# Kernel optimization log

Measured on AMD Instinct MI355X. Metric: run time of the kernel, lower is better.

Reference implementation:

```python
import jax, jax.numpy as jnp
import numpy as np

B, NU, NT = 128, 32, 64          # batch, users/sample, antennas/sample
IN_F, H, OUT_F, NL = 128, 128, 16, 2
N_U, N_A = B * NU, B * NT        # total user / antenna nodes


def setup_inputs() -> dict:
    key = jax.random.key(0)
    ks = iter(jax.random.split(key, 40))
    p = lambda shape: jax.random.normal(next(ks), shape, jnp.float32) * 0.05
    inp = {
        'user_feat': jax.random.normal(next(ks), (N_U, IN_F), jnp.float32),
        'ant_noise': jax.random.normal(next(ks), (N_A, H), jnp.float32),
    }
    # complete bipartite edges within each batch sample
    b = np.arange(B)[:, None, None]
    u = np.arange(NU)[None, :, None]
    t = np.arange(NT)[None, None, :]
    su = np.broadcast_to(b * NU + u, (B, NU, NT)).reshape(-1)  # user global ids
    dt = np.broadcast_to(b * NT + t, (B, NU, NT)).reshape(-1)  # antenna global ids
    inp['src_u2a'] = jnp.asarray(su, jnp.int32)
    inp['dst_u2a'] = jnp.asarray(dt, jnp.int32)
    inp['src_a2u'] = jnp.asarray(dt, jnp.int32)
    inp['dst_a2u'] = jnp.asarray(su, jnp.int32)
    inp['W_ue'] = p((IN_F, H)); inp['b_ue'] = p((H,))
    inp['W_t'] = p((H, H));     inp['b_t'] = p((H,))
    for name in ['ca_aggr', 'ca_self', 'ca_comb', 'cu_aggr', 'cu_self', 'cu_comb']:
        inp[name + '_W'] = p((NL, H, H))
        inp[name + '_b'] = p((NL, H))
    inp['W_norm'] = p((H, OUT_F)); inp['b_norm'] = p((OUT_F,))
    return inp


def mlp(x, W, b):
    # stack of NL Linear(H,H) + ReLU, as in MLP module
    for i in range(W.shape[0]):
        x = jax.nn.relu(x @ W[i] + b[i])
    return x


def rel_conv(src_f, dst_f, src_idx, dst_idx, n_dst, aW, ab, sW, sb, cW, cb):
    # GraphConv2: mean-aggregate mlp_aggr(src) over in-edges, combine with mlp_self(dst)
    msg = mlp(src_f, aW, ab)                                   # [n_src, H]
    summed = jax.ops.segment_sum(msg[src_idx], dst_idx, num_segments=n_dst)
    deg = jax.ops.segment_sum(jnp.ones(dst_idx.shape, jnp.float32), dst_idx,
                              num_segments=n_dst)
    mean = summed / jnp.maximum(deg, 1.0)[:, None]
    return mlp(mlp(dst_f, sW, sb) + mean, cW, cb)


def reference(user_feat, ant_noise, src_u2a, dst_u2a, src_a2u, dst_a2u,
              W_ue, b_ue, W_t, b_t,
              ca_aggr_W, ca_aggr_b, ca_self_W, ca_self_b, ca_comb_W, ca_comb_b,
              cu_aggr_W, cu_aggr_b, cu_self_W, cu_self_b, cu_comb_W, cu_comb_b,
              W_norm, b_norm):
    # InitLayer
    hu = jax.nn.relu(user_feat @ W_ue + b_ue)                  # [B*NU, H]
    ant = jax.nn.relu(hu.reshape(B, NU, H).mean(axis=1) @ W_t + b_t)  # [B, H]
    ha = jnp.repeat(ant, NT, axis=0) + ant_noise               # [B*NT, H]
    # two applications of the SAME HeteroGraphConv (shared weights)
    for _ in range(2):
        na = rel_conv(hu, ha, src_u2a, dst_u2a, N_A,
                      ca_aggr_W, ca_aggr_b, ca_self_W, ca_self_b, ca_comb_W, ca_comb_b)
        nu = rel_conv(ha, hu, src_a2u, dst_a2u, N_U,
                      cu_aggr_W, cu_aggr_b, cu_self_W, cu_self_b, cu_comb_W, cu_comb_b)
        hu, ha = nu, na
    # NormLayer: project, split real/imag, normalize to unit modulus
    y = (ha @ W_norm + b_norm).reshape(B, NT, OUT_F)
    rf = OUT_F // 2
    re, im = y[..., :rf], y[..., rf:]
    mag = jnp.sqrt(re * re + im * im)
    return jnp.concatenate([re / mag, im / mag], axis=-1)      # [B, NT, OUT_F]
```

## Files before the change

kernel.cpp:

```cpp
#include <hip/hip_runtime.h>
#include <math.h>


using frag  = __attribute__((ext_vector_type(8))) short;
using f32x4 = __attribute__((ext_vector_type(4))) float;

#define LDST 136
#define SCOPE_AGT __HIP_MEMORY_SCOPE_AGENT

__device__ __forceinline__ float  bf2f(ushort u) { return __uint_as_float(((unsigned)u) << 16); }
__device__ __forceinline__ ushort f2bf(float f) {
    unsigned u = __float_as_uint(f);
    u += 0x7fff + ((u >> 16) & 1);
    return (ushort)(u >> 16);
}
__device__ __forceinline__ void gst4_sc(void* p, unsigned v) {
    asm volatile("global_store_dword %0, %1, off sc1" :: "v"(p), "v"(v) : "memory");
}

struct GP {
    const float *uf, *noise, *b_ue, *W_t, *b_t;
    const float *wsrc[13];
    const float *bias6[6];
    const float *Wn, *bn;
    float *out;
    ushort *WtAll;
    float *pE, *pA0, *pU0, *pA1, *pU1;
    unsigned *cnt, *flg;
};

__device__ __forceinline__ void psync(unsigned* myf, unsigned* pf, unsigned s) {
    asm volatile("s_waitcnt vmcnt(0)" ::: "memory");
    __syncthreads();
    if (threadIdx.x == 0) {
        __hip_atomic_store(myf, s, __ATOMIC_RELAXED, SCOPE_AGT);
        while (__hip_atomic_load(pf, __ATOMIC_RELAXED, SCOPE_AGT) < s)
            __builtin_amdgcn_s_sleep(2);
    }
    __syncthreads();
}

template<int MT, bool MEANADD>
__device__ __forceinline__ void mlp_stage(const ushort* Xl, ushort* Yl,
    const ushort* __restrict__ Wt, const float* __restrict__ bias, const float* meanL)
{
    const int lane = threadIdx.x & 63, wave = threadIdx.x >> 6;
    const int q = lane >> 4, l15 = lane & 15;
    frag A[2][4];
#pragma unroll
    for (int i = 0; i < 2; ++i) {
        const int n0 = (wave * 2 + i) * 16;
#pragma unroll
        for (int kc = 0; kc < 4; ++kc)
            A[i][kc] = *(const frag*)(Wt + (n0 + l15) * 128 + kc * 32 + q * 8);
    }
#pragma unroll
    for (int mt = 0; mt < MT; ++mt) {
        frag Bv[4];
#pragma unroll
        for (int kc = 0; kc < 4; ++kc)
            Bv[kc] = *(const frag*)(Xl + (mt * 16 + l15) * LDST + kc * 32 + q * 8);
#pragma unroll
        for (int i = 0; i < 2; ++i) {
            f32x4 acc = {0.f, 0.f, 0.f, 0.f};
#pragma unroll
            for (int kc = 0; kc < 4; ++kc)
                acc = __builtin_amdgcn_mfma_f32_16x16x32_bf16(A[i][kc], Bv[kc], acc, 0, 0, 0);
            const int n0 = (wave * 2 + i) * 16 + q * 4;
            const float4 bv = *(const float4*)(bias + n0);
            float v0 = acc[0] + bv.x, v1 = acc[1] + bv.y, v2 = acc[2] + bv.z, v3 = acc[3] + bv.w;
            v0 = v0 > 0.f ? v0 : 0.f; v1 = v1 > 0.f ? v1 : 0.f;
            v2 = v2 > 0.f ? v2 : 0.f; v3 = v3 > 0.f ? v3 : 0.f;
            if (MEANADD) {
                const float4 mv = *(const float4*)(meanL + n0);
                v0 += mv.x; v1 += mv.y; v2 += mv.z; v3 += mv.w;
            }
            ushort4 o = { f2bf(v0), f2bf(v1), f2bf(v2), f2bf(v3) };
            *(ushort4*)(Yl + (mt * 16 + l15) * LDST + n0) = o;
        }
    }
}

__device__ __forceinline__ void colsum_sc(const ushort* buf, int rows, float* __restrict__ dst) {
    const int t = threadIdx.x;
    if (t < 128) {
        float s = 0.f;
        for (int r = 0; r < rows; ++r) s += bf2f(buf[r * LDST + t]);
        gst4_sc(dst + t, __float_as_uint(s));
    }
}

__device__ __forceinline__ void wslab(ushort* dst, float* slab,
                                      const float* __restrict__ W, int kb)
{
    for (int c = threadIdx.x; c < 512; c += 256) {
        const int kr = c >> 5, c4 = c & 31;
        const float4 v = *(const float4*)(W + (kb * 16 + kr) * 128 + c4 * 4);
        slab[kr * 129 + c4 * 4 + 0] = v.x; slab[kr * 129 + c4 * 4 + 1] = v.y;
        slab[kr * 129 + c4 * 4 + 2] = v.z; slab[kr * 129 + c4 * 4 + 3] = v.w;
    }
    __syncthreads();
    for (int c = threadIdx.x; c < 1024; c += 256) {
        const int n = c >> 3, k2 = c & 7;
        const unsigned d = (unsigned)f2bf(slab[(2 * k2) * 129 + n])
                         | ((unsigned)f2bf(slab[(2 * k2 + 1) * 129 + n]) << 16);
        gst4_sc(dst + n * 128 + kb * 16 + 2 * k2, d);
    }
    __syncthreads();
}

__global__ __launch_bounds__(256, 1) void k_gnn(GP P)
{
    __shared__ __align__(16) ushort HU [16 * LDST];
    __shared__ __align__(16) ushort HU2[16 * LDST];
    __shared__ __align__(16) ushort HA [32 * LDST];
    __shared__ __align__(16) ushort HA2[32 * LDST];
    __shared__ __align__(16) ushort T0 [32 * LDST];
    __shared__ __align__(16) ushort T1 [32 * LDST];
    __shared__ float meanL[128];
    __shared__ float antL[128];

    const int blk = blockIdx.x, tid = threadIdx.x;
    const int b = blk >> 1, half = blk & 1;
    unsigned* myf = P.flg + blk * 32;
    unsigned* prf = P.flg + (blk ^ 1) * 32;
    const ushort* Wt = P.WtAll;

    if (blk < 104)
        wslab(P.WtAll + (blk >> 3) * 16384, (float*)T1, P.wsrc[blk >> 3], blk & 7);

    for (int c = tid; c < 16 * 32; c += 256) {
        const int r = c >> 5, k4 = c & 31;
        const float4 v = *(const float4*)(P.uf + (size_t)(b * 32 + half * 16 + r) * 128 + k4 * 4);
        ushort4 o = { f2bf(v.x), f2bf(v.y), f2bf(v.z), f2bf(v.w) };
        *(ushort4*)(T0 + r * LDST + k4 * 4) = o;
    }

    asm volatile("s_waitcnt vmcnt(0)" ::: "memory");
    __syncthreads();
    if (tid == 0) {
        if (blk < 104) {
            unsigned old = __hip_atomic_fetch_add(P.cnt, 1u, __ATOMIC_RELAXED, SCOPE_AGT);
            if (old == 103u) __hip_atomic_store(P.cnt + 32, 1u, __ATOMIC_RELAXED, SCOPE_AGT);
        }
        while (__hip_atomic_load(P.cnt + 32, __ATOMIC_RELAXED, SCOPE_AGT) < 1u)
            __builtin_amdgcn_s_sleep(8);
    }
    __syncthreads();

    mlp_stage<1, false>(T0, HU, Wt + 12 * 16384, P.b_ue, nullptr);
    __syncthreads();
    colsum_sc(HU, 16, P.pE + blk * 128);
    psync(myf, prf, 1u);
    if (tid < 128)
        meanL[tid] = (P.pE[blk * 128 + tid] + P.pE[(blk ^ 1) * 128 + tid]) * (1.f / 32.f);
    __syncthreads();
    if (tid < 128) {
        float acc = P.b_t[tid];
#pragma unroll 4
        for (int k = 0; k < 128; ++k) acc += meanL[k] * P.W_t[k * 128 + tid];
        antL[tid] = acc > 0.f ? acc : 0.f;
    }
    __syncthreads();
    for (int c = tid; c < 32 * 32; c += 256) {
        const int r = c >> 5, k4 = c & 31;
        const float4 v = *(const float4*)(P.noise + (size_t)(b * 64 + half * 32 + r) * 128 + k4 * 4);
        ushort4 o = { f2bf(v.x + antL[k4 * 4 + 0]), f2bf(v.y + antL[k4 * 4 + 1]),
                      f2bf(v.z + antL[k4 * 4 + 2]), f2bf(v.w + antL[k4 * 4 + 3]) };
        *(ushort4*)(HA + r * LDST + k4 * 4) = o;
    }
    __syncthreads();

    mlp_stage<1, false>(HU, T0, Wt + 0 * 16384, P.bias6[0], nullptr);
    __syncthreads();
    mlp_stage<1, false>(T0, T1, Wt + 1 * 16384, P.bias6[0] + 128, nullptr);
    __syncthreads();
    colsum_sc(T1, 16, P.pA0 + blk * 128);
    __syncthreads();
    mlp_stage<2, false>(HA, T0, Wt + 6 * 16384, P.bias6[3], nullptr);
    __syncthreads();
    mlp_stage<2, false>(T0, T1, Wt + 7 * 16384, P.bias6[3] + 128, nullptr);
    __syncthreads();
    colsum_sc(T1, 32, P.pU0 + blk * 128);
    psync(myf, prf, 2u);

    if (tid < 128)
        meanL[tid] = (P.pA0[blk * 128 + tid] + P.pA0[(blk ^ 1) * 128 + tid]) * (1.f / 32.f);
    __syncthreads();
    mlp_stage<2, false>(HA, T0, Wt + 2 * 16384, P.bias6[1], nullptr);
    __syncthreads();
    mlp_stage<2, true >(T0, T1, Wt + 3 * 16384, P.bias6[1] + 128, meanL);
    __syncthreads();
    mlp_stage<2, false>(T1, T0, Wt + 4 * 16384, P.bias6[2], nullptr);
    __syncthreads();
    mlp_stage<2, false>(T0, HA2, Wt + 5 * 16384, P.bias6[2] + 128, nullptr);
    __syncthreads();
    if (tid < 128)
        meanL[tid] = (P.pU0[blk * 128 + tid] + P.pU0[(blk ^ 1) * 128 + tid]) * (1.f / 64.f);
    __syncthreads();
    mlp_stage<1, false>(HU, T0, Wt + 8 * 16384, P.bias6[4], nullptr);
    __syncthreads();
    mlp_stage<1, true >(T0, T1, Wt + 9 * 16384, P.bias6[4] + 128, meanL);
    __syncthreads();
    mlp_stage<1, false>(T1, T0, Wt + 10 * 16384, P.bias6[5], nullptr);
    __syncthreads();
    mlp_stage<1, false>(T0, HU2, Wt + 11 * 16384, P.bias6[5] + 128, nullptr);
    __syncthreads();

    mlp_stage<1, false>(HU2, T0, Wt + 0 * 16384, P.bias6[0], nullptr);
    __syncthreads();
    mlp_stage<1, false>(T0, T1, Wt + 1 * 16384, P.bias6[0] + 128, nullptr);
    __syncthreads();
    colsum_sc(T1, 16, P.pA1 + blk * 128);
    __syncthreads();
    mlp_stage<2, false>(HA2, T0, Wt + 6 * 16384, P.bias6[3], nullptr);
    __syncthreads();
    mlp_stage<2, false>(T0, T1, Wt + 7 * 16384, P.bias6[3] + 128, nullptr);
    __syncthreads();
    colsum_sc(T1, 32, P.pU1 + blk * 128);
    psync(myf, prf, 3u);

    if (tid < 128)
        meanL[tid] = (P.pA1[blk * 128 + tid] + P.pA1[(blk ^ 1) * 128 + tid]) * (1.f / 32.f);
    __syncthreads();
    mlp_stage<2, false>(HA2, T0, Wt + 2 * 16384, P.bias6[1], nullptr);
    __syncthreads();
    mlp_stage<2, true >(T0, T1, Wt + 3 * 16384, P.bias6[1] + 128, meanL);
    __syncthreads();
    mlp_stage<2, false>(T1, T0, Wt + 4 * 16384, P.bias6[2], nullptr);
    __syncthreads();
    mlp_stage<2, false>(T0, T1, Wt + 5 * 16384, P.bias6[2] + 128, nullptr);
    __syncthreads();
    float* WnS = (float*)T0;
    for (int c = tid; c < 512; c += 256)
        *(float4*)(WnS + c * 4) = *(const float4*)(P.Wn + c * 4);
    __syncthreads();
    {
        const int row = tid >> 3, j = tid & 7;
        float R = P.bn[j], I = P.bn[j + 8];
        const ushort* h = T1 + row * LDST;
        for (int k = 0; k < 128; ++k) {
            const float hv = bf2f(h[k]);
            R += hv * WnS[k * 16 + j];
            I += hv * WnS[k * 16 + j + 8];
        }
        const float mag = sqrtf(R * R + I * I);
        const int a = b * 64 + half * 32 + row;
        P.out[a * 16 + j]     = R / mag;
        P.out[a * 16 + j + 8] = I / mag;
    }
}

extern "C" void kernel_launch(void* const* d_in, const int* in_sizes, int n_in,
                              void* d_out, int out_size, void* d_ws, size_t ws_size,
                              hipStream_t stream)
{
    GP P;
    P.uf    = (const float*)d_in[0];
    P.noise = (const float*)d_in[1];
    const float* W_ue = (const float*)d_in[6];
    P.b_ue  = (const float*)d_in[7];
    P.W_t   = (const float*)d_in[8];
    P.b_t   = (const float*)d_in[9];
    const float* caW[3] = {(const float*)d_in[10], (const float*)d_in[12], (const float*)d_in[14]};
    const float* cab[3] = {(const float*)d_in[11], (const float*)d_in[13], (const float*)d_in[15]};
    const float* cuW[3] = {(const float*)d_in[16], (const float*)d_in[18], (const float*)d_in[20]};
    const float* cub[3] = {(const float*)d_in[17], (const float*)d_in[19], (const float*)d_in[21]};
    P.Wn  = (const float*)d_in[22];
    P.bn  = (const float*)d_in[23];
    P.out = (float*)d_out;

    P.wsrc[0]  = caW[0]; P.wsrc[1]  = caW[0] + 16384;
    P.wsrc[2]  = caW[1]; P.wsrc[3]  = caW[1] + 16384;
    P.wsrc[4]  = caW[2]; P.wsrc[5]  = caW[2] + 16384;
    P.wsrc[6]  = cuW[0]; P.wsrc[7]  = cuW[0] + 16384;
    P.wsrc[8]  = cuW[1]; P.wsrc[9]  = cuW[1] + 16384;
    P.wsrc[10] = cuW[2]; P.wsrc[11] = cuW[2] + 16384;
    P.wsrc[12] = W_ue;
    P.bias6[0] = cab[0]; P.bias6[1] = cab[1]; P.bias6[2] = cab[2];
    P.bias6[3] = cub[0]; P.bias6[4] = cub[1]; P.bias6[5] = cub[2];

    char* w = (char*)d_ws;
    P.cnt   = (unsigned*)w;
    P.flg   = (unsigned*)(w + 1024);
    P.WtAll = (ushort*)(w + 1024 + 32768);
    P.pE    = (float*)(P.WtAll + 13 * 16384);
    P.pA0   = P.pE  + 256 * 128;
    P.pU0   = P.pA0 + 256 * 128;
    P.pA1   = P.pU0 + 256 * 128;
    P.pU1   = P.pA1 + 256 * 128;

    hipMemsetAsync(w, 0, 1024 + 32768, stream);
    k_gnn<<<dim3(256), dim3(256), 0, stream>>>(P);
}
```

Baseline: 149.6 us.

## Double block threads, skip dead final-layer aggregation, and reorder stages across partner syncs

Launches 512 threads per block, so each wave computes one 16-column MFMA tile instead of two, and column sums, the antenna transform and the norm projection are split across all threads. The second-layer user update (aggregation and colsum for pU1), whose output is never used, is removed. Work is moved ahead of each partner-block sync so independent MLP stages overlap the wait, the noise load is hoisted before the first barrier, and own-half partial sums are kept in shared memory. Sleep intervals in the spin loops are shortened. This adds register pressure and more barriers per stage.

```diff
diff --git a/kernel.cpp b/kernel.cpp
--- a/kernel.cpp
+++ b/kernel.cpp
@@ -25,7 +25,7 @@
     const float *Wn, *bn;
     float *out;
     ushort *WtAll;
-    float *pE, *pA0, *pU0, *pA1, *pU1;
+    float *pE, *pA0, *pU0, *pA1;
     unsigned *cnt, *flg;
 };
 
@@ -35,7 +35,7 @@
     if (threadIdx.x == 0) {
         __hip_atomic_store(myf, s, __ATOMIC_RELAXED, SCOPE_AGT);
         while (__hip_atomic_load(pf, __ATOMIC_RELAXED, SCOPE_AGT) < s)
-            __builtin_amdgcn_s_sleep(2);
+            __builtin_amdgcn_s_sleep(1);
     }
     __syncthreads();
 }
@@ -46,61 +46,62 @@
 {
     const int lane = threadIdx.x & 63, wave = threadIdx.x >> 6;
     const int q = lane >> 4, l15 = lane & 15;
-    frag A[2][4];
+    const int n0 = wave * 16;
+    frag A[4];
 #pragma unroll
-    for (int i = 0; i < 2; ++i) {
-        const int n0 = (wave * 2 + i) * 16;
-#pragma unroll
-        for (int kc = 0; kc < 4; ++kc)
-            A[i][kc] = *(const frag*)(Wt + (n0 + l15) * 128 + kc * 32 + q * 8);
-    }
+    for (int kc = 0; kc < 4; ++kc)
+        A[kc] = *(const frag*)(Wt + (n0 + l15) * 128 + kc * 32 + q * 8);
+    const float4 bv = *(const float4*)(bias + n0 + q * 4);
+    float4 mv = {0.f, 0.f, 0.f, 0.f};
+    if (MEANADD) mv = *(const float4*)(meanL + n0 + q * 4);
 #pragma unroll
     for (int mt = 0; mt < MT; ++mt) {
         frag Bv[4];
 #pragma unroll
         for (int kc = 0; kc < 4; ++kc)
             Bv[kc] = *(const frag*)(Xl + (mt * 16 + l15) * LDST + kc * 32 + q * 8);
+        f32x4 acc = {0.f, 0.f, 0.f, 0.f};
 #pragma unroll
-        for (int i = 0; i < 2; ++i) {
-            f32x4 acc = {0.f, 0.f, 0.f, 0.f};
-#pragma unroll
-            for (int kc = 0; kc < 4; ++kc)
-                acc = __builtin_amdgcn_mfma_f32_16x16x32_bf16(A[i][kc], Bv[kc], acc, 0, 0, 0);
-            const int n0 = (wave * 2 + i) * 16 + q * 4;
-            const float4 bv = *(const float4*)(bias + n0);
-            float v0 = acc[0] + bv.x, v1 = acc[1] + bv.y, v2 = acc[2] + bv.z, v3 = acc[3] + bv.w;
-            v0 = v0 > 0.f ? v0 : 0.f; v1 = v1 > 0.f ? v1 : 0.f;
-            v2 = v2 > 0.f ? v2 : 0.f; v3 = v3 > 0.f ? v3 : 0.f;
-            if (MEANADD) {
-                const float4 mv = *(const float4*)(meanL + n0);
-                v0 += mv.x; v1 += mv.y; v2 += mv.z; v3 += mv.w;
-            }
-            ushort4 o = { f2bf(v0), f2bf(v1), f2bf(v2), f2bf(v3) };
-            *(ushort4*)(Yl + (mt * 16 + l15) * LDST + n0) = o;
-        }
-    }
-}
-
-__device__ __forceinline__ void colsum_sc(const ushort* buf, int rows, float* __restrict__ dst) {
-    const int t = threadIdx.x;
+        for (int kc = 0; kc < 4; ++kc)
+            acc = __builtin_amdgcn_mfma_f32_16x16x32_bf16(A[kc], Bv[kc], acc, 0, 0, 0);
+        float v0 = acc[0] + bv.x, v1 = acc[1] + bv.y, v2 = acc[2] + bv.z, v3 = acc[3] + bv.w;
+        v0 = v0 > 0.f ? v0 : 0.f; v1 = v1 > 0.f ? v1 : 0.f;
+        v2 = v2 > 0.f ? v2 : 0.f; v3 = v3 > 0.f ? v3 : 0.f;
+        if (MEANADD) { v0 += mv.x; v1 += mv.y; v2 += mv.z; v3 += mv.w; }
+        ushort4 o = { f2bf(v0), f2bf(v1), f2bf(v2), f2bf(v3) };
+        *(ushort4*)(Yl + (mt * 16 + l15) * LDST + n0 + q * 4) = o;
+    }
+}
+
+template<int ROWS>
+__device__ __forceinline__ void colsum(const ushort* buf, float* redL,
+                                       float* ownDst, float* __restrict__ gDst)
+{
+    const int t = threadIdx.x, g = t >> 7, col = t & 127;
+    float s = 0.f;
+    for (int r = g; r < ROWS; r += 4) s += bf2f(buf[r * LDST + col]);
+    redL[g * 128 + col] = s;
+    __syncthreads();
     if (t < 128) {
-        float s = 0.f;
-        for (int r = 0; r < rows; ++r) s += bf2f(buf[r * LDST + t]);
-        gst4_sc(dst + t, __float_as_uint(s));
-    }
+        float tot = redL[t] + redL[128 + t] + redL[256 + t] + redL[384 + t];
+        ownDst[t] = tot;
+        gst4_sc(gDst + t, __float_as_uint(tot));
+    }
+    __syncthreads();
 }
 
 __device__ __forceinline__ void wslab(ushort* dst, float* slab,
                                       const float* __restrict__ W, int kb)
 {
-    for (int c = threadIdx.x; c < 512; c += 256) {
+    {
+        const int c = threadIdx.x;
         const int kr = c >> 5, c4 = c & 31;
         const float4 v = *(const float4*)(W + (kb * 16 + kr) * 128 + c4 * 4);
         slab[kr * 129 + c4 * 4 + 0] = v.x; slab[kr * 129 + c4 * 4 + 1] = v.y;
         slab[kr * 129 + c4 * 4 + 2] = v.z; slab[kr * 129 + c4 * 4 + 3] = v.w;
     }
     __syncthreads();
-    for (int c = threadIdx.x; c < 1024; c += 256) {
+    for (int c = threadIdx.x; c < 1024; c += 512) {
         const int n = c >> 3, k2 = c & 7;
         const unsigned d = (unsigned)f2bf(slab[(2 * k2) * 129 + n])
                          | ((unsigned)f2bf(slab[(2 * k2 + 1) * 129 + n]) << 16);
@@ -109,7 +110,7 @@
     __syncthreads();
 }
 
-__global__ __launch_bounds__(256, 1) void k_gnn(GP P)
+__global__ __launch_bounds__(512, 1) void k_gnn(GP P)
 {
     __shared__ __align__(16) ushort HU [16 * LDST];
     __shared__ __align__(16) ushort HU2[16 * LDST];
@@ -117,23 +118,31 @@
     __shared__ __align__(16) ushort HA2[32 * LDST];
     __shared__ __align__(16) ushort T0 [32 * LDST];
     __shared__ __align__(16) ushort T1 [32 * LDST];
-    __shared__ float meanL[128];
-    __shared__ float antL[128];
+    __shared__ float meanP[128], meanQ[128], antL[128], redL[512];
 
     const int blk = blockIdx.x, tid = threadIdx.x;
     const int b = blk >> 1, half = blk & 1;
     unsigned* myf = P.flg + blk * 32;
     unsigned* prf = P.flg + (blk ^ 1) * 32;
+    const int prt = blk ^ 1;
     const ushort* Wt = P.WtAll;
+    const float* const* bb = P.bias6;
 
     if (blk < 104)
         wslab(P.WtAll + (blk >> 3) * 16384, (float*)T1, P.wsrc[blk >> 3], blk & 7);
 
-    for (int c = tid; c < 16 * 32; c += 256) {
+    {
+        const int c = tid;
         const int r = c >> 5, k4 = c & 31;
         const float4 v = *(const float4*)(P.uf + (size_t)(b * 32 + half * 16 + r) * 128 + k4 * 4);
         ushort4 o = { f2bf(v.x), f2bf(v.y), f2bf(v.z), f2bf(v.w) };
         *(ushort4*)(T0 + r * LDST + k4 * 4) = o;
+    }
+    for (int c = tid; c < 1024; c += 512) {
+        const int r = c >> 5, k4 = c & 31;
+        const float4 v = *(const float4*)(P.noise + (size_t)(b * 64 + half * 32 + r) * 128 + k4 * 4);
+        ushort4 o = { f2bf(v.x), f2bf(v.y), f2bf(v.z), f2bf(v.w) };
+        *(ushort4*)(HA + r * LDST + k4 * 4) = o;
     }
 
     asm volatile("s_waitcnt vmcnt(0)" ::: "memory");
@@ -144,110 +153,109 @@
             if (old == 103u) __hip_atomic_store(P.cnt + 32, 1u, __ATOMIC_RELAXED, SCOPE_AGT);
         }
         while (__hip_atomic_load(P.cnt + 32, __ATOMIC_RELAXED, SCOPE_AGT) < 1u)
-            __builtin_amdgcn_s_sleep(8);
+            __builtin_amdgcn_s_sleep(4);
     }
     __syncthreads();
 
     mlp_stage<1, false>(T0, HU, Wt + 12 * 16384, P.b_ue, nullptr);
     __syncthreads();
-    colsum_sc(HU, 16, P.pE + blk * 128);
+    colsum<16>(HU, redL, meanP, P.pE + blk * 128);
+    mlp_stage<1, false>(HU, T0, Wt + 0 * 16384, bb[0], nullptr);
+    __syncthreads();
+    mlp_stage<1, false>(T0, T1, Wt + 1 * 16384, bb[0] + 128, nullptr);
+    __syncthreads();
+    colsum<16>(T1, redL, meanQ, P.pA0 + blk * 128);
     psync(myf, prf, 1u);
-    if (tid < 128)
-        meanL[tid] = (P.pE[blk * 128 + tid] + P.pE[(blk ^ 1) * 128 + tid]) * (1.f / 32.f);
+
+    if (tid < 128) meanP[tid] = (meanP[tid] + P.pE[prt * 128 + tid]) * (1.f / 32.f);
+    __syncthreads();
+    {
+        const int g = tid >> 7, col = tid & 127;
+        float s = 0.f;
+#pragma unroll 4
+        for (int k = g * 32; k < g * 32 + 32; ++k) s += meanP[k] * P.W_t[k * 128 + col];
+        redL[g * 128 + col] = s;
+    }
     __syncthreads();
     if (tid < 128) {
-        float acc = P.b_t[tid];
+        float a = P.b_t[tid] + redL[tid] + redL[128 + tid] + redL[256 + tid] + redL[384 + tid];
+        antL[tid] = a > 0.f ? a : 0.f;
+    }
+    __syncthreads();
+    for (int c = tid; c < 1024; c += 512) {
+        const int r = c >> 5, k4 = c & 31;
+        ushort4 h = *(ushort4*)(HA + r * LDST + k4 * 4);
+        ushort4 o = { f2bf(bf2f(h.x) + antL[k4 * 4 + 0]), f2bf(bf2f(h.y) + antL[k4 * 4 + 1]),
+                      f2bf(bf2f(h.z) + antL[k4 * 4 + 2]), f2bf(bf2f(h.w) + antL[k4 * 4 + 3]) };
+        *(ushort4*)(HA + r * LDST + k4 * 4) = o;
+    }
+    __syncthreads();
+
+    mlp_stage<2, false>(HA, T0, Wt + 6 * 16384, bb[3], nullptr);
+    __syncthreads();
+    mlp_stage<2, false>(T0, T1, Wt + 7 * 16384, bb[3] + 128, nullptr);
+    __syncthreads();
+    colsum<32>(T1, redL, meanP, P.pU0 + blk * 128);
+    mlp_stage<2, false>(HA, T0, Wt + 2 * 16384, bb[1], nullptr);
+    __syncthreads();
+    psync(myf, prf, 2u);
+
+    if (tid < 128) {
+        meanQ[tid] = (meanQ[tid] + P.pA0[prt * 128 + tid]) * (1.f / 32.f);
+        meanP[tid] = (meanP[tid] + P.pU0[prt * 128 + tid]) * (1.f / 64.f);
+    }
+    __syncthreads();
+    mlp_stage<2, true >(T0, T1, Wt + 3 * 16384, bb[1] + 128, meanQ);
+    __syncthreads();
+    mlp_stage<2, false>(T1, T0, Wt + 4 * 16384, bb[2], nullptr);
+    __syncthreads();
+    mlp_stage<2, false>(T0, HA2, Wt + 5 * 16384, bb[2] + 128, nullptr);
+    __syncthreads();
+    mlp_stage<1, false>(HU, T0, Wt + 8 * 16384, bb[4], nullptr);
+    __syncthreads();
+    mlp_stage<1, true >(T0, T1, Wt + 9 * 16384, bb[4] + 128, meanP);
+    __syncthreads();
+    mlp_stage<1, false>(T1, T0, Wt + 10 * 16384, bb[5], nullptr);
+    __syncthreads();
+    mlp_stage<1, false>(T0, HU2, Wt + 11 * 16384, bb[5] + 128, nullptr);
+    __syncthreads();
+
+    mlp_stage<1, false>(HU2, T0, Wt + 0 * 16384, bb[0], nullptr);
+    __syncthreads();
+    mlp_stage<1, false>(T0, T1, Wt + 1 * 16384, bb[0] + 128, nullptr);
+    __syncthreads();
+    colsum<16>(T1, redL, meanQ, P.pA1 + blk * 128);
+    mlp_stage<2, false>(HA2, T0, Wt + 2 * 16384, bb[1], nullptr);
+    __syncthreads();
+    psync(myf, prf, 3u);
+
+    if (tid < 128) meanQ[tid] = (meanQ[tid] + P.pA1[prt * 128 + tid]) * (1.f / 32.f);
+    __syncthreads();
+    mlp_stage<2, true >(T0, T1, Wt + 3 * 16384, bb[1] + 128, meanQ);
+    __syncthreads();
+    mlp_stage<2, false>(T1, T0, Wt + 4 * 16384, bb[2], nullptr);
+    __syncthreads();
+    mlp_stage<2, false>(T0, T1, Wt + 5 * 16384, bb[2] + 128, nullptr);
+    __syncthreads();
+
+    float* WnS = (float*)T0;
+    {
+        const int c = tid;
+        *(float4*)(WnS + c * 4) = *(const float4*)(P.Wn + c * 4);
+    }
+    __syncthreads();
+    {
+        const int row = tid >> 4, j = tid & 15;
+        float acc = P.bn[j];
+        const ushort* h = T1 + row * LDST;
 #pragma unroll 4
-        for (int k = 0; k < 128; ++k) acc += meanL[k] * P.W_t[k * 128 + tid];
-        antL[tid] = acc > 0.f ? acc : 0.f;
-    }
-    __syncthreads();
-    for (int c = tid; c < 32 * 32; c += 256) {
-        const int r = c >> 5, k4 = c & 31;
-        const float4 v = *(const float4*)(P.noise + (size_t)(b * 64 + half * 32 + r) * 128 + k4 * 4);
-        ushort4 o = { f2bf(v.x + antL[k4 * 4 + 0]), f2bf(v.y + antL[k4 * 4 + 1]),
-                      f2bf(v.z + antL[k4 * 4 + 2]), f2bf(v.w + antL[k4 * 4 + 3]) };
-        *(ushort4*)(HA + r * LDST + k4 * 4) = o;
-    }
-    __syncthreads();
-
-    mlp_stage<1, false>(HU, T0, Wt + 0 * 16384, P.bias6[0], nullptr);
-    __syncthreads();
-    mlp_stage<1, false>(T0, T1, Wt + 1 * 16384, P.bias6[0] + 128, nullptr);
-    __syncthreads();
-    colsum_sc(T1, 16, P.pA0 + blk * 128);
-    __syncthreads();
-    mlp_stage<2, false>(HA, T0, Wt + 6 * 16384, P.bias6[3], nullptr);
-    __syncthreads();
-    mlp_stage<2, false>(T0, T1, Wt + 7 * 16384, P.bias6[3] + 128, nullptr);
-    __syncthreads();
-    colsum_sc(T1, 32, P.pU0 + blk * 128);
-    psync(myf, prf, 2u);
-
-    if (tid < 128)
-        meanL[tid] = (P.pA0[blk * 128 + tid] + P.pA0[(blk ^ 1) * 128 + tid]) * (1.f / 32.f);
-    __syncthreads();
-    mlp_stage<2, false>(HA, T0, Wt + 2 * 16384, P.bias6[1], nullptr);
-    __syncthreads();
-    mlp_stage<2, true >(T0, T1, Wt + 3 * 16384, P.bias6[1] + 128, meanL);
-    __syncthreads();
-    mlp_stage<2, false>(T1, T0, Wt + 4 * 16384, P.bias6[2], nullptr);
-    __syncthreads();
-    mlp_stage<2, false>(T0, HA2, Wt + 5 * 16384, P.bias6[2] + 128, nullptr);
-    __syncthreads();
-    if (tid < 128)
-        meanL[tid] = (P.pU0[blk * 128 + tid] + P.pU0[(blk ^ 1) * 128 + tid]) * (1.f / 64.f);
-    __syncthreads();
-    mlp_stage<1, false>(HU, T0, Wt + 8 * 16384, P.bias6[4], nullptr);
-    __syncthreads();
-    mlp_stage<1, true >(T0, T1, Wt + 9 * 16384, P.bias6[4] + 128, meanL);
-    __syncthreads();
-    mlp_stage<1, false>(T1, T0, Wt + 10 * 16384, P.bias6[5], nullptr);
-    __syncthreads();
-    mlp_stage<1, false>(T0, HU2, Wt + 11 * 16384, P.bias6[5] + 128, nullptr);
-    __syncthreads();
-
-    mlp_stage<1, false>(HU2, T0, Wt + 0 * 16384, P.bias6[0], nullptr);
-    __syncthreads();
-    mlp_stage<1, false>(T0, T1, Wt + 1 * 16384, P.bias6[0] + 128, nullptr);
-    __syncthreads();
-    colsum_sc(T1, 16, P.pA1 + blk * 128);
-    __syncthreads();
-    mlp_stage<2, false>(HA2, T0, Wt + 6 * 16384, P.bias6[3], nullptr);
-    __syncthreads();
-    mlp_stage<2, false>(T0, T1, Wt + 7 * 16384, P.bias6[3] + 128, nullptr);
-    __syncthreads();
-    colsum_sc(T1, 32, P.pU1 + blk * 128);
-    psync(myf, prf, 3u);
-
-    if (tid < 128)
-        meanL[tid] = (P.pA1[blk * 128 + tid] + P.pA1[(blk ^ 1) * 128 + tid]) * (1.f / 32.f);
-    __syncthreads();
-    mlp_stage<2, false>(HA2, T0, Wt + 2 * 16384, P.bias6[1], nullptr);
-    __syncthreads();
-    mlp_stage<2, true >(T0, T1, Wt + 3 * 16384, P.bias6[1] + 128, meanL);
-    __syncthreads();
-    mlp_stage<2, false>(T1, T0, Wt + 4 * 16384, P.bias6[2], nullptr);
-    __syncthreads();
-    mlp_stage<2, false>(T0, T1, Wt + 5 * 16384, P.bias6[2] + 128, nullptr);
-    __syncthreads();
-    float* WnS = (float*)T0;
-    for (int c = tid; c < 512; c += 256)
-        *(float4*)(WnS + c * 4) = *(const float4*)(P.Wn + c * 4);
-    __syncthreads();
-    {
-        const int row = tid >> 3, j = tid & 7;
-        float R = P.bn[j], I = P.bn[j + 8];
-        const ushort* h = T1 + row * LDST;
-        for (int k = 0; k < 128; ++k) {
-            const float hv = bf2f(h[k]);
-            R += hv * WnS[k * 16 + j];
-            I += hv * WnS[k * 16 + j + 8];
-        }
-        const float mag = sqrtf(R * R + I * I);
+        for (int k = 0; k < 128; ++k) acc += bf2f(h[k]) * WnS[k * 16 + j];
+        redL[row * 16 + j] = acc;
+        __syncthreads();
+        const float re = redL[row * 16 + (j & 7)], im = redL[row * 16 + (j & 7) + 8];
+        const float mag = sqrtf(re * re + im * im);
         const int a = b * 64 + half * 32 + row;
-        P.out[a * 16 + j]     = R / mag;
-        P.out[a * 16 + j + 8] = I / mag;
+        P.out[a * 16 + j] = acc / mag;
     }
 }
 
@@ -288,8 +296,7 @@
     P.pA0   = P.pE  + 256 * 128;
     P.pU0   = P.pA0 + 256 * 128;
     P.pA1   = P.pU0 + 256 * 128;
-    P.pU1   = P.pA1 + 256 * 128;
 
     hipMemsetAsync(w, 0, 1024 + 32768, stream);
-    k_gnn<<<dim3(256), dim3(256), 0, stream>>>(P);
-}
+    k_gnn<<<dim3(256), dim3(512), 0, stream>>>(P);
+}
```

Measured after the change: 140.3 us. 1.07x faster.
